# Performance work log

Hardware: AMD Instinct MI355X
Metric: run time of the kernel (lower is better)

The kernel has to match this reference:

```python
import jax, jax.numpy as jnp
import numpy as np

D, H, DOUT, E, B = 1024, 4096, 1024, 8, 8192
TOP_K = 2


def setup_inputs() -> dict:
    key = jax.random.key(0)
    ks = jax.random.split(key, 12)
    s = 0.02
    return {
        "x": jax.random.normal(ks[0], (B, D), jnp.float32),
        # stacked expert params: Linear(D,H) -> ReLU -> Linear(H,H//2) -> ReLU -> Linear(H//2,DOUT)
        "W1": jax.random.normal(ks[1], (E, D, H), jnp.float32) * s,
        "b1": jnp.zeros((E, H), jnp.float32),
        "W2": jax.random.normal(ks[2], (E, H, H // 2), jnp.float32) * s,
        "b2": jnp.zeros((E, H // 2), jnp.float32),
        "W3": jax.random.normal(ks[3], (E, H // 2, DOUT), jnp.float32) * s,
        "b3": jnp.zeros((E, DOUT), jnp.float32),
        # gate: Linear(D, D//2) -> ReLU -> Linear(D//2, E) -> Softmax
        "Wg1": jax.random.normal(ks[4], (D, D // 2), jnp.float32) * s,
        "bg1": jnp.zeros((D // 2,), jnp.float32),
        "Wg2": jax.random.normal(ks[5], (D // 2, E), jnp.float32) * s,
        "bg2": jnp.zeros((E,), jnp.float32),
    }


def reference(x, W1, b1, W2, b2, W3, b3, Wg1, bg1, Wg2, bg2):
    # inference-mode math: dropout identity, no gate noise (training=False)
    num_experts = W1.shape[0]
    # gate weights: softmax over experts, [B, E]
    g = jax.nn.relu(x @ Wg1 + bg1)
    gate_weights = jax.nn.softmax(g @ Wg2 + bg2, axis=-1)
    # top-k routing, renormalized with softmax over selected logits
    top_w, top_idx = jax.lax.top_k(gate_weights, TOP_K)  # [B, k]
    top_w = jax.nn.softmax(top_w, axis=-1)
    # dense all-expert MLPs (as the original does): [E, B, *]
    h1 = jax.nn.relu(jnp.einsum("bd,edh->ebh", x, W1) + b1[:, None, :])
    h2 = jax.nn.relu(jnp.einsum("ebh,ehm->ebm", h1, W2) + b2[:, None, :])
    eo = jnp.einsum("ebm,emo->ebo", h2, W3) + b3[:, None, :]  # [E, B, DOUT]
    eo = jnp.swapaxes(eo, 0, 1)  # [B, E, DOUT]
    # gather top-k expert outputs and combine
    sel = jnp.take_along_axis(eo, top_idx[:, :, None], axis=1)  # [B, k, DOUT]
    final_output = jnp.sum(top_w[:, :, None] * sel, axis=1)  # [B, DOUT]
    # load balance loss on the (pre-topk) gate distribution
    expert_usage = jnp.mean(gate_weights, axis=0)
    load_balance_loss = jnp.mean((expert_usage - 1.0 / num_experts) ** 2)
    return final_output, load_balance_loss
```

## Files before the change

kernel.cpp:

```cpp
#include <hip/hip_runtime.h>

#define B_ROWS 8192
#define DDIM 1024
#define HDIM 4096
#define H2DIM 2048
#define DOUT_N 1024
#define NEXP 8
#define ROW_TILES 136
#define PAD_ROWS (ROW_TILES*128)

typedef __attribute__((ext_vector_type(8))) short short8;
typedef __attribute__((ext_vector_type(4))) float f32x4;

__device__ inline unsigned short f2bf(float f) {
  unsigned int u = __builtin_bit_cast(unsigned int, f);
  u += 0x7fffu + ((u >> 16) & 1u);
  return (unsigned short)(u >> 16);
}

__device__ inline void gld_lds16(const void* g, void* l) {
  __builtin_amdgcn_global_load_lds(
      (const __attribute__((address_space(1))) void*)g,
      (__attribute__((address_space(3))) void*)l, 16, 0, 0);
}

#define WAITV(N) asm volatile("s_waitcnt vmcnt(" #N ")" ::: "memory")

__device__ inline void barrier_raw() {
  asm volatile("" ::: "memory");
  __builtin_amdgcn_s_barrier();
  asm volatile("" ::: "memory");
}

__global__ __launch_bounds__(256) void gate1_kernel(
    const float* __restrict__ x, const float* __restrict__ Wg1,
    const float* __restrict__ bg1, float* __restrict__ g) {
  __shared__ float a_s[16][132];
  __shared__ float b_s[16][64];
  const int t = threadIdx.x;
  const int row0 = blockIdx.y * 128;
  const int n0 = blockIdx.x * 64;
  const int tx = t & 15, ty = t >> 4;
  float c[8][4] = {};
  const int la_row = t >> 2, la_kq = (t & 3) * 4;
  const int lb_kk = t >> 4, lb_c = (t & 15) * 4;
  for (int k0 = 0; k0 < DDIM; k0 += 16) {
#pragma unroll
    for (int i = 0; i < 2; ++i) {
      int row = la_row + i * 64;
      float4 av = *(const float4*)&x[(size_t)(row0 + row) * DDIM + k0 + la_kq];
      a_s[la_kq + 0][row] = av.x; a_s[la_kq + 1][row] = av.y;
      a_s[la_kq + 2][row] = av.z; a_s[la_kq + 3][row] = av.w;
    }
    *(float4*)&b_s[lb_kk][lb_c] = *(const float4*)&Wg1[(size_t)(k0 + lb_kk) * 512 + n0 + lb_c];
    __syncthreads();
#pragma unroll
    for (int kk = 0; kk < 16; ++kk) {
      float4 b4 = *(const float4*)&b_s[kk][tx * 4];
      float4 a4lo = *(const float4*)&a_s[kk][ty * 8];
      float4 a4hi = *(const float4*)&a_s[kk][ty * 8 + 4];
      float aa[8] = {a4lo.x, a4lo.y, a4lo.z, a4lo.w, a4hi.x, a4hi.y, a4hi.z, a4hi.w};
      float bb[4] = {b4.x, b4.y, b4.z, b4.w};
#pragma unroll
      for (int i = 0; i < 8; ++i)
#pragma unroll
        for (int j = 0; j < 4; ++j) c[i][j] += aa[i] * bb[j];
    }
    __syncthreads();
  }
  float bb[4];
#pragma unroll
  for (int j = 0; j < 4; ++j) bb[j] = bg1[n0 + tx * 4 + j];
#pragma unroll
  for (int i = 0; i < 8; ++i) {
    float4 v;
    v.x = fmaxf(c[i][0] + bb[0], 0.f);
    v.y = fmaxf(c[i][1] + bb[1], 0.f);
    v.z = fmaxf(c[i][2] + bb[2], 0.f);
    v.w = fmaxf(c[i][3] + bb[3], 0.f);
    *(float4*)&g[(size_t)(row0 + ty * 8 + i) * 512 + n0 + tx * 4] = v;
  }
}

__global__ __launch_bounds__(256) void gate2_kernel(
    const float* __restrict__ g, const float* __restrict__ Wg2,
    const float* __restrict__ bg2, int* __restrict__ top_idx,
    float* __restrict__ top_w, int* __restrict__ counts,
    float* __restrict__ usage) {
  __shared__ float w2t[NEXP * 512];
  __shared__ float us[NEXP];
  __shared__ int cs[NEXP];
  const int t = threadIdx.x;
  for (int i = t; i < NEXP * 512; i += 256) {
    int k = i >> 3, e = i & 7;
    w2t[e * 512 + k] = Wg2[i];
  }
  if (t < NEXP) { us[t] = 0.f; cs[t] = 0; }
  __syncthreads();
  const int lane = t & 63, wid = t >> 6;
  const int row = blockIdx.x * 4 + wid;
  float part[NEXP] = {};
  const float* grow = &g[(size_t)row * 512];
#pragma unroll
  for (int j = 0; j < 8; ++j) {
    int k = lane + j * 64;
    float gv = grow[k];
#pragma unroll
    for (int e = 0; e < NEXP; ++e) part[e] += gv * w2t[e * 512 + k];
  }
#pragma unroll
  for (int e = 0; e < NEXP; ++e)
    for (int m = 32; m >= 1; m >>= 1) part[e] += __shfl_xor(part[e], m);
  if (lane == 0) {
    float p[NEXP];
    float mx = -1e30f;
#pragma unroll
    for (int e = 0; e < NEXP; ++e) { p[e] = part[e] + bg2[e]; mx = fmaxf(mx, p[e]); }
    float s = 0.f;
#pragma unroll
    for (int e = 0; e < NEXP; ++e) { p[e] = expf(p[e] - mx); s += p[e]; }
    float inv = 1.f / s;
#pragma unroll
    for (int e = 0; e < NEXP; ++e) { p[e] *= inv; atomicAdd(&us[e], p[e]); }
    int i0 = 0; float b0 = p[0];
    for (int e = 1; e < NEXP; ++e) if (p[e] > b0) { b0 = p[e]; i0 = e; }
    int i1 = -1; float b1 = -1.f;
    for (int e = 0; e < NEXP; ++e) {
      if (e == i0) continue;
      if (p[e] > b1) { b1 = p[e]; i1 = e; }
    }
    float e1 = expf(b1 - b0);
    float w0 = 1.f / (1.f + e1);
    top_idx[row * 2 + 0] = i0; top_idx[row * 2 + 1] = i1;
    top_w[row * 2 + 0] = w0;   top_w[row * 2 + 1] = e1 * w0;
    atomicAdd(&cs[i0], 1); atomicAdd(&cs[i1], 1);
  }
  __syncthreads();
  if (t < NEXP) { atomicAdd(&usage[t], us[t]); atomicAdd(&counts[t], cs[t]); }
}

__global__ void offsets_kernel(const int* __restrict__ counts, int* __restrict__ off) {
  if (threadIdx.x == 0) {
    int acc = 0;
    off[0] = 0;
    for (int e = 0; e < NEXP; ++e) {
      acc += (counts[e] + 127) & ~127;
      off[e + 1] = acc;
    }
  }
}

__global__ __launch_bounds__(256) void scatter_kernel(
    const int* __restrict__ top_idx, const int* __restrict__ off,
    int* __restrict__ fill, int* __restrict__ entry, int* __restrict__ posof) {
  int row = blockIdx.x * 256 + threadIdx.x;
#pragma unroll
  for (int k = 0; k < 2; ++k) {
    int e = top_idx[row * 2 + k];
    int pos = atomicAdd(&fill[e], 1);
    entry[off[e] + pos] = row * 2 + k;
    posof[row * 2 + k] = off[e] + pos;
  }
}

__global__ __launch_bounds__(256) void gather_kernel(
    const float* __restrict__ x, const int* __restrict__ entry,
    unsigned short* __restrict__ Xg) {
  const int r = blockIdx.x;
  const int s = entry[r];
  const int t = threadIdx.x;
  unsigned long long packed = 0ull;
  if (s >= 0) {
    float4 f = *(const float4*)&x[(size_t)(s >> 1) * DDIM + t * 4];
    packed = (unsigned long long)f2bf(f.x) |
             ((unsigned long long)f2bf(f.y) << 16) |
             ((unsigned long long)f2bf(f.z) << 32) |
             ((unsigned long long)f2bf(f.w) << 48);
  }
  *(unsigned long long*)&Xg[(size_t)r * DDIM + t * 4] = packed;
}

__global__ __launch_bounds__(256) void transpose_kernel(
    const float* __restrict__ src, unsigned short* __restrict__ dst,
    int K, int N) {
  __shared__ float tile[64][65];
  const size_t eoff = (size_t)blockIdx.z * K * N;
  const int k0 = blockIdx.y * 64, n0 = blockIdx.x * 64;
  const int t = threadIdx.x;
#pragma unroll
  for (int i = 0; i < 16; ++i) {
    int idx = t + i * 256;
    int kk = idx >> 6, nn = idx & 63;
    tile[kk][nn] = src[eoff + (size_t)(k0 + kk) * N + n0 + nn];
  }
  __syncthreads();
#pragma unroll
  for (int i = 0; i < 16; ++i) {
    int idx = t + i * 256;
    int nn = idx >> 6, kk = idx & 63;
    dst[eoff + (size_t)(n0 + nn) * K + k0 + kk] = f2bf(tile[kk][nn]);
  }
}

template <int KDIM, int EPI>
__global__ __launch_bounds__(512, 2) void expert_gemm(
    const unsigned short* __restrict__ A, const unsigned short* __restrict__ Bt,
    const float* __restrict__ bias, unsigned short* __restrict__ Cout,
    float* __restrict__ Eo, const int* __restrict__ off, int N) {
  constexpr int NS = KDIM / 32;
  static_assert(NS >= 4, "need >=4 K sub-tiles");
  __shared__ unsigned short smem[4 * 12288];

  const int gx = gridDim.x;
  const int nwg = gx * gridDim.y;
  const int orig = blockIdx.x + gx * blockIdx.y;
  const int cpx = nwg >> 3;
  const int swz = (orig & 7) * cpx + (orig >> 3);
  const int tm = swz / gx, tn = swz - tm * gx;
  const int tileM = tm * 128;
  if (tileM >= off[NEXP]) return;
  int e = 0;
  while (e < NEXP - 1 && off[e + 1] <= tileM) ++e;
  const int tileN = tn * 256;

  const int t = threadIdx.x;
  const int lane = t & 63, wid = t >> 6;
  const int wr = (wid >> 2) * 64;
  const int wc = (wid & 3) * 64;
  const int l16 = lane & 15, q = lane >> 4;

  const unsigned short* Abase = A + (size_t)tileM * KDIM;
  const unsigned short* Bbase = Bt + ((size_t)e * N + tileN) * (size_t)KDIM;

  const int srow0 = wid * 16 + (lane >> 2);
  const int scp = lane & 3;

  f32x4 acc[4][4];
#pragma unroll
  for (int i = 0; i < 4; ++i)
#pragma unroll
    for (int j = 0; j < 4; ++j) acc[i][j] = (f32x4){0.f, 0.f, 0.f, 0.f};

  auto stage = [&](int s) {
    unsigned short* buf = &smem[(size_t)(s & 3) * 12288];
    const int k0 = s * 32;
    {
      const int row = srow0;
      const int c = scp ^ ((row >> 1) & 3);
      gld_lds16(Abase + (size_t)row * KDIM + k0 + c * 8,
                buf + (size_t)(wid * 16) * 32);
    }
#pragma unroll
    for (int j = 0; j < 2; ++j) {
      const int row = j * 128 + srow0;
      const int c = scp ^ ((row >> 1) & 3);
      gld_lds16(Bbase + (size_t)row * KDIM + k0 + c * 8,
                buf + 4096 + (size_t)(j * 128 + wid * 16) * 32);
    }
  };

  auto rdfrags = [&](int s, short8* af, short8* bf) {
    const unsigned short* buf = &smem[(size_t)(s & 3) * 12288];
#pragma unroll
    for (int i = 0; i < 4; ++i) {
      const int row = wr + 16 * i + l16;
      const int c = q ^ ((row >> 1) & 3);
      af[i] = *(const short8*)&buf[row * 32 + c * 8];
    }
#pragma unroll
    for (int j = 0; j < 4; ++j) {
      const int row = wc + 16 * j + l16;
      const int c = q ^ ((row >> 1) & 3);
      bf[j] = *(const short8*)&buf[4096 + row * 32 + c * 8];
    }
  };

  auto domfma = [&](short8* af, short8* bf) {
    __builtin_amdgcn_s_setprio(1);
#pragma unroll
    for (int i = 0; i < 4; ++i)
#pragma unroll
      for (int j = 0; j < 4; ++j)
        acc[i][j] = __builtin_amdgcn_mfma_f32_16x16x32_bf16(af[i], bf[j], acc[i][j], 0, 0, 0);
    __builtin_amdgcn_s_setprio(0);
  };

  stage(0); stage(1); stage(2);
  WAITV(6);
  barrier_raw();

#pragma unroll 4
  for (int s = 0; s < NS - 3; ++s) {
    short8 af[4], bf[4];
    rdfrags(s, af, bf);
    stage(s + 3);
    domfma(af, bf);
    WAITV(6);
    barrier_raw();
  }
  {
    short8 af[4], bf[4];
    rdfrags(NS - 3, af, bf);
    domfma(af, bf);
    WAITV(3);
    barrier_raw();
  }
  {
    short8 af[4], bf[4];
    rdfrags(NS - 2, af, bf);
    domfma(af, bf);
    WAITV(0);
    barrier_raw();
  }
  {
    short8 af[4], bf[4];
    rdfrags(NS - 1, af, bf);
    domfma(af, bf);
  }

  if (EPI == 0) {
#pragma unroll
    for (int j = 0; j < 4; ++j) {
      const int gCol = tileN + wc + 16 * j + l16;
      const float bcol = bias[e * N + gCol];
#pragma unroll
      for (int i = 0; i < 4; ++i) {
        const int gRow0 = tileM + wr + 16 * i + q * 4;
#pragma unroll
        for (int r = 0; r < 4; ++r)
          Cout[(size_t)(gRow0 + r) * N + gCol] = f2bf(fmaxf(acc[i][j][r] + bcol, 0.f));
      }
    }
  } else {
    float bcol[4];
#pragma unroll
    for (int j = 0; j < 4; ++j) bcol[j] = bias[e * N + tileN + wc + 16 * j + l16];
#pragma unroll
    for (int i = 0; i < 4; ++i) {
      const int gRow0 = tileM + wr + 16 * i + q * 4;
#pragma unroll
      for (int r = 0; r < 4; ++r) {
        float* orow = Eo + (size_t)(gRow0 + r) * N;
#pragma unroll
        for (int j = 0; j < 4; ++j)
          orow[tileN + wc + 16 * j + l16] = acc[i][j][r] + bcol[j];
      }
    }
  }
}

__global__ __launch_bounds__(256) void combine_kernel(
    const float* __restrict__ eo, const int* __restrict__ posof,
    const float* __restrict__ tw, float* __restrict__ out) {
  const int row = blockIdx.x;
  const int c = threadIdx.x * 4;
  const int p0 = posof[row * 2 + 0], p1 = posof[row * 2 + 1];
  const float w0 = tw[row * 2 + 0], w1 = tw[row * 2 + 1];
  float4 a = *(const float4*)&eo[(size_t)p0 * DOUT_N + c];
  float4 b = *(const float4*)&eo[(size_t)p1 * DOUT_N + c];
  float4 o;
  o.x = w0 * a.x + w1 * b.x;
  o.y = w0 * a.y + w1 * b.y;
  o.z = w0 * a.z + w1 * b.z;
  o.w = w0 * a.w + w1 * b.w;
  *(float4*)&out[(size_t)row * DOUT_N + c] = o;
}

__global__ void loss_kernel(const float* __restrict__ usage, float* __restrict__ out) {
  if (threadIdx.x == 0) {
    float l = 0.f;
    for (int e = 0; e < NEXP; ++e) {
      float d = usage[e] * (1.f / B_ROWS) - 1.f / NEXP;
      l += d * d;
    }
    out[(size_t)B_ROWS * DOUT_N] = l * (1.f / NEXP);
  }
}

extern "C" void kernel_launch(void* const* d_in, const int* in_sizes, int n_in,
                              void* d_out, int out_size, void* d_ws, size_t ws_size,
                              hipStream_t stream) {
  (void)in_sizes; (void)n_in; (void)ws_size;
  const float* x   = (const float*)d_in[0];
  const float* W1  = (const float*)d_in[1];
  const float* b1  = (const float*)d_in[2];
  const float* W2  = (const float*)d_in[3];
  const float* b2  = (const float*)d_in[4];
  const float* W3  = (const float*)d_in[5];
  const float* b3  = (const float*)d_in[6];
  const float* Wg1 = (const float*)d_in[7];
  const float* bg1 = (const float*)d_in[8];
  const float* Wg2 = (const float*)d_in[9];
  const float* bg2 = (const float*)d_in[10];
  float* out = (float*)d_out;

  char* ws = (char*)d_ws;
  size_t p = 0;
  auto alloc = [&](size_t bytes) {
    void* r = ws + p;
    p = (p + bytes + 255) & ~(size_t)255;
    return r;
  };
  int*   off    = (int*)alloc(9 * 4);
  int*   counts = (int*)alloc(NEXP * 4);
  int*   fill   = (int*)alloc(NEXP * 4);
  float* usage  = (float*)alloc(NEXP * 4);
  int*   tidx   = (int*)alloc((size_t)B_ROWS * 2 * 4);
  float* tw     = (float*)alloc((size_t)B_ROWS * 2 * 4);
  int*   posof  = (int*)alloc((size_t)B_ROWS * 2 * 4);
  int*   entry  = (int*)alloc((size_t)PAD_ROWS * 4);
  float* g      = (float*)alloc((size_t)B_ROWS * 512 * 4);
  unsigned short* Xg  = (unsigned short*)alloc((size_t)PAD_ROWS * DDIM * 2);
  unsigned short* W1t = (unsigned short*)alloc((size_t)NEXP * HDIM * DDIM * 2);
  unsigned short* W2t = (unsigned short*)alloc((size_t)NEXP * H2DIM * HDIM * 2);
  unsigned short* W3t = (unsigned short*)alloc((size_t)NEXP * DOUT_N * H2DIM * 2);
  unsigned short* h1  = (unsigned short*)alloc((size_t)PAD_ROWS * HDIM * 2);
  unsigned short* h2  = (unsigned short*)alloc((size_t)PAD_ROWS * H2DIM * 2);
  float* eo = (float*)h1;

  hipMemsetAsync(d_out, 0, (size_t)out_size * 4, stream);
  hipMemsetAsync(counts, 0, NEXP * 4, stream);
  hipMemsetAsync(fill, 0, NEXP * 4, stream);
  hipMemsetAsync(usage, 0, NEXP * 4, stream);
  hipMemsetAsync(entry, 0xFF, (size_t)PAD_ROWS * 4, stream);

  transpose_kernel<<<dim3(HDIM / 64, DDIM / 64, NEXP), 256, 0, stream>>>(W1, W1t, DDIM, HDIM);
  transpose_kernel<<<dim3(H2DIM / 64, HDIM / 64, NEXP), 256, 0, stream>>>(W2, W2t, HDIM, H2DIM);
  transpose_kernel<<<dim3(DOUT_N / 64, H2DIM / 64, NEXP), 256, 0, stream>>>(W3, W3t, H2DIM, DOUT_N);

  gate1_kernel<<<dim3(512 / 64, B_ROWS / 128), 256, 0, stream>>>(x, Wg1, bg1, g);
  gate2_kernel<<<B_ROWS / 4, 256, 0, stream>>>(g, Wg2, bg2, tidx, tw, counts, usage);
  offsets_kernel<<<1, 64, 0, stream>>>(counts, off);
  scatter_kernel<<<B_ROWS / 256, 256, 0, stream>>>(tidx, off, fill, entry, posof);
  gather_kernel<<<PAD_ROWS, 256, 0, stream>>>(x, entry, Xg);

  expert_gemm<DDIM, 0><<<dim3(HDIM / 256, ROW_TILES), 512, 0, stream>>>(
      Xg, W1t, b1, h1, nullptr, off, HDIM);
  expert_gemm<HDIM, 0><<<dim3(H2DIM / 256, ROW_TILES), 512, 0, stream>>>(
      h1, W2t, b2, h2, nullptr, off, H2DIM);
  expert_gemm<H2DIM, 1><<<dim3(DOUT_N / 256, ROW_TILES), 512, 0, stream>>>(
      h2, W3t, b3, nullptr, eo, off, DOUT_N);
  combine_kernel<<<B_ROWS, 256, 0, stream>>>(eo, posof, tw, out);

  loss_kernel<<<1, 64, 0, stream>>>(usage, out);
}
```

Measured before the change: 1.492 ms.

## Enlarge expert GEMM tiles to 256 rows with 3-stage split pipeline

The expert GEMM moves from 128-row to 256-row M tiles, with each wave computing two 64-row halves. It uses a 3-buffer LDS pipeline whose A and B prefetches are split around two MFMA phases, and the last GEMM gets a narrower N tile. Expert padding becomes 256 rows to match, h2 reuses the Xg buffer, and the gate1 and weight-transpose kernels are widened with vectorized loads and stores. The goal is more operand reuse per LDS load and fewer redundant weight reads. The cost is higher register pressure from 8xNF accumulators and extra padded rows per expert.

```diff
diff --git a/kernel.cpp b/kernel.cpp
--- a/kernel.cpp
+++ b/kernel.cpp
@@ -6,8 +6,8 @@
 #define H2DIM 2048
 #define DOUT_N 1024
 #define NEXP 8
-#define ROW_TILES 136
-#define PAD_ROWS (ROW_TILES*128)
+#define ROW_TILES 72
+#define PAD_ROWS (ROW_TILES*256)
 
 typedef __attribute__((ext_vector_type(8))) short short8;
 typedef __attribute__((ext_vector_type(4))) float f32x4;
@@ -35,50 +35,60 @@
 __global__ __launch_bounds__(256) void gate1_kernel(
     const float* __restrict__ x, const float* __restrict__ Wg1,
     const float* __restrict__ bg1, float* __restrict__ g) {
-  __shared__ float a_s[16][132];
-  __shared__ float b_s[16][64];
+  __shared__ float a_s[16][136];
+  __shared__ float b_s[16][128];
   const int t = threadIdx.x;
   const int row0 = blockIdx.y * 128;
-  const int n0 = blockIdx.x * 64;
+  const int n0 = blockIdx.x * 128;
   const int tx = t & 15, ty = t >> 4;
-  float c[8][4] = {};
-  const int la_row = t >> 2, la_kq = (t & 3) * 4;
-  const int lb_kk = t >> 4, lb_c = (t & 15) * 4;
+  float c[8][8] = {};
+  const int la_row = t >> 1, la_k = (t & 1) * 8;
+  const int lb_k = t >> 4, lb_c = (t & 15) * 8;
   for (int k0 = 0; k0 < DDIM; k0 += 16) {
-#pragma unroll
-    for (int i = 0; i < 2; ++i) {
-      int row = la_row + i * 64;
-      float4 av = *(const float4*)&x[(size_t)(row0 + row) * DDIM + k0 + la_kq];
-      a_s[la_kq + 0][row] = av.x; a_s[la_kq + 1][row] = av.y;
-      a_s[la_kq + 2][row] = av.z; a_s[la_kq + 3][row] = av.w;
-    }
-    *(float4*)&b_s[lb_kk][lb_c] = *(const float4*)&Wg1[(size_t)(k0 + lb_kk) * 512 + n0 + lb_c];
+    float4 av0 = *(const float4*)&x[(size_t)(row0 + la_row) * DDIM + k0 + la_k];
+    float4 av1 = *(const float4*)&x[(size_t)(row0 + la_row) * DDIM + k0 + la_k + 4];
+    a_s[la_k + 0][la_row] = av0.x; a_s[la_k + 1][la_row] = av0.y;
+    a_s[la_k + 2][la_row] = av0.z; a_s[la_k + 3][la_row] = av0.w;
+    a_s[la_k + 4][la_row] = av1.x; a_s[la_k + 5][la_row] = av1.y;
+    a_s[la_k + 6][la_row] = av1.z; a_s[la_k + 7][la_row] = av1.w;
+    *(float4*)&b_s[lb_k][lb_c]     = *(const float4*)&Wg1[(size_t)(k0 + lb_k) * 512 + n0 + lb_c];
+    *(float4*)&b_s[lb_k][lb_c + 4] = *(const float4*)&Wg1[(size_t)(k0 + lb_k) * 512 + n0 + lb_c + 4];
     __syncthreads();
 #pragma unroll
     for (int kk = 0; kk < 16; ++kk) {
-      float4 b4 = *(const float4*)&b_s[kk][tx * 4];
-      float4 a4lo = *(const float4*)&a_s[kk][ty * 8];
-      float4 a4hi = *(const float4*)&a_s[kk][ty * 8 + 4];
-      float aa[8] = {a4lo.x, a4lo.y, a4lo.z, a4lo.w, a4hi.x, a4hi.y, a4hi.z, a4hi.w};
-      float bb[4] = {b4.x, b4.y, b4.z, b4.w};
+      float4 b0 = *(const float4*)&b_s[kk][tx * 4];
+      float4 b1 = *(const float4*)&b_s[kk][64 + tx * 4];
+      float4 a0 = *(const float4*)&a_s[kk][ty * 8];
+      float4 a1 = *(const float4*)&a_s[kk][ty * 8 + 4];
+      float aa[8] = {a0.x, a0.y, a0.z, a0.w, a1.x, a1.y, a1.z, a1.w};
+      float bb[8] = {b0.x, b0.y, b0.z, b0.w, b1.x, b1.y, b1.z, b1.w};
 #pragma unroll
       for (int i = 0; i < 8; ++i)
 #pragma unroll
-        for (int j = 0; j < 4; ++j) c[i][j] += aa[i] * bb[j];
+        for (int j = 0; j < 8; ++j) c[i][j] += aa[i] * bb[j];
     }
     __syncthreads();
   }
-  float bb[4];
-#pragma unroll
-  for (int j = 0; j < 4; ++j) bb[j] = bg1[n0 + tx * 4 + j];
+  float bb[8];
+#pragma unroll
+  for (int j = 0; j < 4; ++j) {
+    bb[j] = bg1[n0 + tx * 4 + j];
+    bb[4 + j] = bg1[n0 + 64 + tx * 4 + j];
+  }
 #pragma unroll
   for (int i = 0; i < 8; ++i) {
-    float4 v;
-    v.x = fmaxf(c[i][0] + bb[0], 0.f);
-    v.y = fmaxf(c[i][1] + bb[1], 0.f);
-    v.z = fmaxf(c[i][2] + bb[2], 0.f);
-    v.w = fmaxf(c[i][3] + bb[3], 0.f);
-    *(float4*)&g[(size_t)(row0 + ty * 8 + i) * 512 + n0 + tx * 4] = v;
+    float4 v0, v1;
+    v0.x = fmaxf(c[i][0] + bb[0], 0.f);
+    v0.y = fmaxf(c[i][1] + bb[1], 0.f);
+    v0.z = fmaxf(c[i][2] + bb[2], 0.f);
+    v0.w = fmaxf(c[i][3] + bb[3], 0.f);
+    v1.x = fmaxf(c[i][4] + bb[4], 0.f);
+    v1.y = fmaxf(c[i][5] + bb[5], 0.f);
+    v1.z = fmaxf(c[i][6] + bb[6], 0.f);
+    v1.w = fmaxf(c[i][7] + bb[7], 0.f);
+    const size_t ro = (size_t)(row0 + ty * 8 + i) * 512;
+    *(float4*)&g[ro + n0 + tx * 4] = v0;
+    *(float4*)&g[ro + n0 + 64 + tx * 4] = v1;
   }
 }
 
@@ -144,7 +154,7 @@
     int acc = 0;
     off[0] = 0;
     for (int e = 0; e < NEXP; ++e) {
-      acc += (counts[e] + 127) & ~127;
+      acc += (counts[e] + 255) & ~255;
       off[e + 1] = acc;
     }
   }
@@ -187,29 +197,36 @@
   const size_t eoff = (size_t)blockIdx.z * K * N;
   const int k0 = blockIdx.y * 64, n0 = blockIdx.x * 64;
   const int t = threadIdx.x;
-#pragma unroll
-  for (int i = 0; i < 16; ++i) {
-    int idx = t + i * 256;
-    int kk = idx >> 6, nn = idx & 63;
-    tile[kk][nn] = src[eoff + (size_t)(k0 + kk) * N + n0 + nn];
+  const int lr = t >> 4, lc = (t & 15) * 4;
+#pragma unroll
+  for (int r = 0; r < 4; ++r) {
+    const int kk = lr + r * 16;
+    float4 v = *(const float4*)&src[eoff + (size_t)(k0 + kk) * N + n0 + lc];
+    tile[kk][lc] = v.x; tile[kk][lc + 1] = v.y;
+    tile[kk][lc + 2] = v.z; tile[kk][lc + 3] = v.w;
   }
   __syncthreads();
 #pragma unroll
-  for (int i = 0; i < 16; ++i) {
-    int idx = t + i * 256;
-    int nn = idx >> 6, kk = idx & 63;
-    dst[eoff + (size_t)(n0 + nn) * K + k0 + kk] = f2bf(tile[kk][nn]);
-  }
-}
-
-template <int KDIM, int EPI>
+  for (int r = 0; r < 4; ++r) {
+    const int nn = lr + r * 16;
+    ushort4 o;
+    o.x = f2bf(tile[lc + 0][nn]); o.y = f2bf(tile[lc + 1][nn]);
+    o.z = f2bf(tile[lc + 2][nn]); o.w = f2bf(tile[lc + 3][nn]);
+    *(ushort4*)&dst[eoff + (size_t)(n0 + nn) * K + k0 + lc] = o;
+  }
+}
+
+template <int KDIM, int NF, int EPI>
 __global__ __launch_bounds__(512, 2) void expert_gemm(
     const unsigned short* __restrict__ A, const unsigned short* __restrict__ Bt,
     const float* __restrict__ bias, unsigned short* __restrict__ Cout,
     float* __restrict__ Eo, const int* __restrict__ off, int N) {
   constexpr int NS = KDIM / 32;
+  constexpr int BN = NF * 64;
+  constexpr int BUFA = 8192;
+  constexpr int SSTR = BUFA + BN * 32;
   static_assert(NS >= 4, "need >=4 K sub-tiles");
-  __shared__ unsigned short smem[4 * 12288];
+  __shared__ unsigned short smem[3 * SSTR];
 
   const int gx = gridDim.x;
   const int nwg = gx * gridDim.y;
@@ -217,114 +234,117 @@
   const int cpx = nwg >> 3;
   const int swz = (orig & 7) * cpx + (orig >> 3);
   const int tm = swz / gx, tn = swz - tm * gx;
-  const int tileM = tm * 128;
+  const int tileM = tm * 256;
   if (tileM >= off[NEXP]) return;
   int e = 0;
   while (e < NEXP - 1 && off[e + 1] <= tileM) ++e;
-  const int tileN = tn * 256;
+  const int tileN = tn * BN;
 
   const int t = threadIdx.x;
   const int lane = t & 63, wid = t >> 6;
-  const int wr = (wid >> 2) * 64;
-  const int wc = (wid & 3) * 64;
+  const int wr = (wid >> 2) * 128;
+  const int wc = (wid & 3) * (NF * 16);
   const int l16 = lane & 15, q = lane >> 4;
 
   const unsigned short* Abase = A + (size_t)tileM * KDIM;
   const unsigned short* Bbase = Bt + ((size_t)e * N + tileN) * (size_t)KDIM;
 
-  const int srow0 = wid * 16 + (lane >> 2);
-  const int scp = lane & 3;
-
-  f32x4 acc[4][4];
-#pragma unroll
-  for (int i = 0; i < 4; ++i)
-#pragma unroll
-    for (int j = 0; j < 4; ++j) acc[i][j] = (f32x4){0.f, 0.f, 0.f, 0.f};
-
-  auto stage = [&](int s) {
-    unsigned short* buf = &smem[(size_t)(s & 3) * 12288];
-    const int k0 = s * 32;
-    {
-      const int row = srow0;
-      const int c = scp ^ ((row >> 1) & 3);
+  const int srow = t >> 2;
+  const int sch = t & 3;
+  const int ldsw = wid * 512;
+
+  f32x4 acc[8][NF];
+#pragma unroll
+  for (int i = 0; i < 8; ++i)
+#pragma unroll
+    for (int j = 0; j < NF; ++j) acc[i][j] = (f32x4){0.f, 0.f, 0.f, 0.f};
+
+  auto stageA = [&](int k0, int dst) {
+#pragma unroll
+    for (int r = 0; r < 2; ++r) {
+      const int row = r * 128 + srow;
+      const int c = sch ^ ((row >> 1) & 3);
       gld_lds16(Abase + (size_t)row * KDIM + k0 + c * 8,
-                buf + (size_t)(wid * 16) * 32);
-    }
-#pragma unroll
-    for (int j = 0; j < 2; ++j) {
-      const int row = j * 128 + srow0;
-      const int c = scp ^ ((row >> 1) & 3);
+                &smem[dst + r * 4096 + ldsw]);
+    }
+  };
+  auto stageB = [&](int k0, int dst) {
+#pragma unroll
+    for (int r = 0; r < NF / 2; ++r) {
+      const int row = r * 128 + srow;
+      const int c = sch ^ ((row >> 1) & 3);
       gld_lds16(Bbase + (size_t)row * KDIM + k0 + c * 8,
-                buf + 4096 + (size_t)(j * 128 + wid * 16) * 32);
+                &smem[dst + BUFA + r * 4096 + ldsw]);
     }
   };
 
-  auto rdfrags = [&](int s, short8* af, short8* bf) {
-    const unsigned short* buf = &smem[(size_t)(s & 3) * 12288];
+  auto rd_a = [&](const unsigned short* buf, int half, short8* af) {
 #pragma unroll
     for (int i = 0; i < 4; ++i) {
-      const int row = wr + 16 * i + l16;
+      const int row = wr + half * 64 + 16 * i + l16;
       const int c = q ^ ((row >> 1) & 3);
       af[i] = *(const short8*)&buf[row * 32 + c * 8];
     }
-#pragma unroll
-    for (int j = 0; j < 4; ++j) {
+  };
+  auto rd_b = [&](const unsigned short* buf, short8* bf) {
+#pragma unroll
+    for (int j = 0; j < NF; ++j) {
       const int row = wc + 16 * j + l16;
       const int c = q ^ ((row >> 1) & 3);
-      bf[j] = *(const short8*)&buf[4096 + row * 32 + c * 8];
+      bf[j] = *(const short8*)&buf[BUFA + row * 32 + c * 8];
     }
   };
 
-  auto domfma = [&](short8* af, short8* bf) {
+  stageA(0, 0); stageB(0, 0);
+  stageA(32, SSTR); stageB(32, SSTR);
+  if constexpr (NF == 4) WAITV(4); else WAITV(3);
+  barrier_raw();
+
+  int co = 0, so = 2 * SSTR;
+  short8 bf[NF];
+  for (int s = 0; s < NS; ++s) {
+    const unsigned short* buf = &smem[co];
+    const int kpre = (s + 2) * 32;
+    short8 af[4];
+    rd_a(buf, 0, af);
+    rd_b(buf, bf);
+    if (s + 2 < NS) stageA(kpre, so);
+    barrier_raw();
     __builtin_amdgcn_s_setprio(1);
 #pragma unroll
     for (int i = 0; i < 4; ++i)
 #pragma unroll
-      for (int j = 0; j < 4; ++j)
+      for (int j = 0; j < NF; ++j)
         acc[i][j] = __builtin_amdgcn_mfma_f32_16x16x32_bf16(af[i], bf[j], acc[i][j], 0, 0, 0);
     __builtin_amdgcn_s_setprio(0);
-  };
-
-  stage(0); stage(1); stage(2);
-  WAITV(6);
-  barrier_raw();
-
-#pragma unroll 4
-  for (int s = 0; s < NS - 3; ++s) {
-    short8 af[4], bf[4];
-    rdfrags(s, af, bf);
-    stage(s + 3);
-    domfma(af, bf);
-    WAITV(6);
     barrier_raw();
-  }
-  {
-    short8 af[4], bf[4];
-    rdfrags(NS - 3, af, bf);
-    domfma(af, bf);
-    WAITV(3);
+    rd_a(buf, 1, af);
+    if (s + 2 < NS) {
+      stageB(kpre, so);
+      if constexpr (NF == 4) WAITV(4); else WAITV(3);
+    } else if (s == NS - 2) {
+      WAITV(0);
+    }
     barrier_raw();
-  }
-  {
-    short8 af[4], bf[4];
-    rdfrags(NS - 2, af, bf);
-    domfma(af, bf);
-    WAITV(0);
+    __builtin_amdgcn_s_setprio(1);
+#pragma unroll
+    for (int i = 0; i < 4; ++i)
+#pragma unroll
+      for (int j = 0; j < NF; ++j)
+        acc[4 + i][j] = __builtin_amdgcn_mfma_f32_16x16x32_bf16(af[i], bf[j], acc[4 + i][j], 0, 0, 0);
+    __builtin_amdgcn_s_setprio(0);
     barrier_raw();
-  }
-  {
-    short8 af[4], bf[4];
-    rdfrags(NS - 1, af, bf);
-    domfma(af, bf);
+    co += SSTR; if (co == 3 * SSTR) co = 0;
+    so += SSTR; if (so == 3 * SSTR) so = 0;
   }
 
   if (EPI == 0) {
 #pragma unroll
-    for (int j = 0; j < 4; ++j) {
+    for (int j = 0; j < NF; ++j) {
       const int gCol = tileN + wc + 16 * j + l16;
       const float bcol = bias[e * N + gCol];
 #pragma unroll
-      for (int i = 0; i < 4; ++i) {
+      for (int i = 0; i < 8; ++i) {
         const int gRow0 = tileM + wr + 16 * i + q * 4;
 #pragma unroll
         for (int r = 0; r < 4; ++r)
@@ -332,17 +352,17 @@
       }
     }
   } else {
-    float bcol[4];
-#pragma unroll
-    for (int j = 0; j < 4; ++j) bcol[j] = bias[e * N + tileN + wc + 16 * j + l16];
-#pragma unroll
-    for (int i = 0; i < 4; ++i) {
+    float bcol[NF];
+#pragma unroll
+    for (int j = 0; j < NF; ++j) bcol[j] = bias[e * N + tileN + wc + 16 * j + l16];
+#pragma unroll
+    for (int i = 0; i < 8; ++i) {
       const int gRow0 = tileM + wr + 16 * i + q * 4;
 #pragma unroll
       for (int r = 0; r < 4; ++r) {
         float* orow = Eo + (size_t)(gRow0 + r) * N;
 #pragma unroll
-        for (int j = 0; j < 4; ++j)
+        for (int j = 0; j < NF; ++j)
           orow[tileN + wc + 16 * j + l16] = acc[i][j][r] + bcol[j];
       }
     }
@@ -415,7 +435,7 @@
   unsigned short* W2t = (unsigned short*)alloc((size_t)NEXP * H2DIM * HDIM * 2);
   unsigned short* W3t = (unsigned short*)alloc((size_t)NEXP * DOUT_N * H2DIM * 2);
   unsigned short* h1  = (unsigned short*)alloc((size_t)PAD_ROWS * HDIM * 2);
-  unsigned short* h2  = (unsigned short*)alloc((size_t)PAD_ROWS * H2DIM * 2);
+  unsigned short* h2 = Xg;
   float* eo = (float*)h1;
 
   hipMemsetAsync(d_out, 0, (size_t)out_size * 4, stream);
@@ -428,17 +448,17 @@
   transpose_kernel<<<dim3(H2DIM / 64, HDIM / 64, NEXP), 256, 0, stream>>>(W2, W2t, HDIM, H2DIM);
   transpose_kernel<<<dim3(DOUT_N / 64, H2DIM / 64, NEXP), 256, 0, stream>>>(W3, W3t, H2DIM, DOUT_N);
 
-  gate1_kernel<<<dim3(512 / 64, B_ROWS / 128), 256, 0, stream>>>(x, Wg1, bg1, g);
+  gate1_kernel<<<dim3(512 / 128, B_ROWS / 128), 256, 0, stream>>>(x, Wg1, bg1, g);
   gate2_kernel<<<B_ROWS / 4, 256, 0, stream>>>(g, Wg2, bg2, tidx, tw, counts, usage);
   offsets_kernel<<<1, 64, 0, stream>>>(counts, off);
   scatter_kernel<<<B_ROWS / 256, 256, 0, stream>>>(tidx, off, fill, entry, posof);
   gather_kernel<<<PAD_ROWS, 256, 0, stream>>>(x, entry, Xg);
 
-  expert_gemm<DDIM, 0><<<dim3(HDIM / 256, ROW_TILES), 512, 0, stream>>>(
+  expert_gemm<DDIM, 4, 0><<<dim3(HDIM / 256, ROW_TILES), 512, 0, stream>>>(
       Xg, W1t, b1, h1, nullptr, off, HDIM);
-  expert_gemm<HDIM, 0><<<dim3(H2DIM / 256, ROW_TILES), 512, 0, stream>>>(
+  expert_gemm<HDIM, 4, 0><<<dim3(H2DIM / 256, ROW_TILES), 512, 0, stream>>>(
       h1, W2t, b2, h2, nullptr, off, H2DIM);
-  expert_gemm<H2DIM, 1><<<dim3(DOUT_N / 256, ROW_TILES), 512, 0, stream>>>(
+  expert_gemm<H2DIM, 2, 1><<<dim3(DOUT_N / 128, ROW_TILES), 512, 0, stream>>>(
       h2, W3t, b3, nullptr, eo, off, DOUT_N);
   combine_kernel<<<B_ROWS, 256, 0, stream>>>(eo, posof, tw, out);
 
```

Measured after the change: 1.504 ms. About the same (+0.8%).
